# Kernel optimization log

Measured on AMD Instinct MI355X. Metric: run time of the kernel, lower is better.

Reference implementation:

```python
import jax, jax.numpy as jnp
import numpy as np

N_NODES = 100000
DIN = 512
B = 1024
T_STEPS = 6
DOUT = 512


def setup_inputs() -> dict:
    key = jax.random.key(0)
    ks = jax.random.split(key, 8)
    s = 0.02  # small init scale for numerical sanity
    x = jax.random.normal(ks[0], (N_NODES, DIN), jnp.float32)
    batch = jnp.sort(jax.random.randint(ks[1], (N_NODES,), 0, B)).astype(jnp.int64)
    Wih = jax.random.normal(ks[2], (4 * DIN, 2 * DIN), jnp.float32) * s
    Whh = jax.random.normal(ks[3], (4 * DIN, DIN), jnp.float32) * s
    bih = jax.random.normal(ks[4], (4 * DIN,), jnp.float32) * s
    bhh = jax.random.normal(ks[5], (4 * DIN,), jnp.float32) * s
    Wpost = jax.random.normal(ks[6], (DOUT, 2 * DIN), jnp.float32) * s
    bpost = jax.random.normal(ks[7], (DOUT,), jnp.float32) * s
    return {"x": x, "batch": batch, "Wih": Wih, "Whh": Whh, "bih": bih,
            "bhh": bhh, "Wpost": Wpost, "bpost": bpost, "num_graphs": B}


def reference(x, batch, Wih, Whh, bih, bhh, Wpost, bpost, num_graphs):
    din = x.shape[1]
    Bg = num_graphs
    h = jnp.zeros((Bg, din), x.dtype)
    c = jnp.zeros((Bg, din), x.dtype)
    q_star = jnp.zeros((Bg, 2 * din), x.dtype)  # [q, r]
    for _ in range(T_STEPS):
        # single-layer LSTM cell over the "batch of graphs" axis
        z = q_star @ Wih.T + h @ Whh.T + (bih + bhh)  # [B, 4*din]
        i, f, g, o = jnp.split(z, 4, axis=-1)  # torch gate order i,f,g,o
        c = jax.nn.sigmoid(f) * c + jax.nn.sigmoid(i) * jnp.tanh(g)
        h = jax.nn.sigmoid(o) * jnp.tanh(c)
        q = h  # [B, din]
        # segment (scatter) softmax attention over nodes of each graph
        e = jnp.sum(x * q[batch], axis=-1)  # [N]
        emax = jax.ops.segment_max(e, batch, num_segments=Bg)
        ex = jnp.exp(e - emax[batch])
        denom = jax.ops.segment_sum(ex, batch, num_segments=Bg)
        a = ex / denom[batch]  # [N]
        r = jax.ops.segment_sum(a[:, None] * x, batch, num_segments=Bg)  # [B, din]
        q_star = jnp.concatenate([q, r], axis=-1)
    # post_pool: Linear(2*din -> dim_out) + bias + ReLU (dropout=0, eval mode)
    out = jax.nn.relu(q_star @ Wpost.T + bpost)
    return out
```

## Files before the change

### kernel.cpp

```cpp
#include <hip/hip_runtime.h>
#include <stdint.h>
#include <stddef.h>

#define DIN    512
#define BGR    1024
#define NGATE  2048
#define KQ     1024
#define DOUT   512
#define TSTEPS 6

typedef unsigned short ushort_t;
typedef short bf16x8 __attribute__((ext_vector_type(8)));
typedef unsigned short u16x8 __attribute__((ext_vector_type(8)));
typedef float f32x4 __attribute__((ext_vector_type(4)));

__device__ __forceinline__ float b2f(unsigned short u) {
    unsigned int i = ((unsigned int)u) << 16;
    float f;
    __builtin_memcpy(&f, &i, 4);
    return f;
}

__device__ __forceinline__ unsigned short f2b(float f) {
    unsigned int i;
    __builtin_memcpy(&i, &f, 4);
    unsigned int lsb = (i >> 16) & 1u;
    i += 0x7fffu + lsb;
    return (unsigned short)(i >> 16);
}

__device__ __forceinline__ float fast_sigmoid(float v) {
    return 1.f / (1.f + __expf(-v));
}

__device__ __forceinline__ float fast_tanh(float v) {
    float t = fabsf(v);
    float e = __expf(-2.f * t);
    float r = (1.f - e) / (1.f + e);
    return v < 0.f ? -r : r;
}

__global__ void probe_dtypes(const ushort_t* x, const ushort_t* Wih,
                             const ushort_t* Whh, const ushort_t* bih,
                             const ushort_t* bhh, const ushort_t* Wpost,
                             const ushort_t* bpost, int* flags)
{
    __shared__ int cnt[7];
    const int tid = threadIdx.x;
    if (tid < 7) cnt[tid] = 0;
    __syncthreads();
    const int t = tid >> 5;
    const int l = tid & 31;
    if (t < 7) {
        const ushort_t* p = (t == 0) ? x : (t == 1) ? Wih : (t == 2) ? Whh
                          : (t == 3) ? bih : (t == 4) ? bhh
                          : (t == 5) ? Wpost : bpost;
        int good = 0;
        for (int i = 0; i < 4; i++) {
            ushort_t u = p[(l * 4 + i) * 2];
            int ex = (u >> 7) & 0xFF;
            if (ex == 0 || (ex >= 96 && ex <= 143)) good++;
        }
        atomicAdd(&cnt[t], good);
    }
    __syncthreads();
    if (tid < 7) flags[tid] = (cnt[tid] < 96) ? 1 : 0;
}

#define BM 64
#define BN 64
#define BK 32

__global__ __launch_bounds__(256)
void gemm_cell(const ushort_t* __restrict__ Ag,
               const ushort_t* __restrict__ Wg,
               const float* __restrict__ bias2,
               float* __restrict__ c, float* __restrict__ H)
{
    __shared__ __align__(16) ushort_t As[BM * BK];
    __shared__ __align__(16) ushort_t Bs[BM * BK];

    const int tid  = threadIdx.x;
    const int lane = tid & 63;
    const int w    = tid >> 6;
    const int lrow = lane & 15;
    const int quad = lane >> 4;

    const int n0 = blockIdx.x * 64;
    const int m0 = blockIdx.y * BM;

    const int srow = tid >> 2;
    const int scol = (tid & 3) * 8;

    const ushort_t* aSrc = Ag + (size_t)(m0 + srow) * KQ + scol;
    const ushort_t* bSrc = Wg + (size_t)(n0 + srow) * KQ + scol;

    f32x4 acc[4];
#pragma unroll
    for (int ni = 0; ni < 4; ni++) acc[ni] = (f32x4){0.f, 0.f, 0.f, 0.f};

    bf16x8 av = *(const bf16x8*)(aSrc);
    bf16x8 bv = *(const bf16x8*)(bSrc);

    for (int kt = 0; kt < KQ; kt += BK) {
        __syncthreads();
        *(bf16x8*)&As[srow * BK + scol] = av;
        *(bf16x8*)&Bs[srow * BK + scol] = bv;
        if (kt + BK < KQ) {
            av = *(const bf16x8*)(aSrc + kt + BK);
            bv = *(const bf16x8*)(bSrc + kt + BK);
        }
        __syncthreads();

        bf16x8 af = *(const bf16x8*)&As[(w * 16 + lrow) * BK + quad * 8];
        bf16x8 bfr[4];
#pragma unroll
        for (int ni = 0; ni < 4; ni++)
            bfr[ni] = *(const bf16x8*)&Bs[(ni * 16 + lrow) * BK + quad * 8];
#pragma unroll
        for (int ni = 0; ni < 4; ni++)
            acc[ni] = __builtin_amdgcn_mfma_f32_16x16x32_bf16(
                af, bfr[ni], acc[ni], 0, 0, 0);
    }

    const int d   = blockIdx.x * 16 + lrow;
    const float bi = bias2[n0 + lrow];
    const float bf = bias2[n0 + 16 + lrow];
    const float bg = bias2[n0 + 32 + lrow];
    const float bo = bias2[n0 + 48 + lrow];
#pragma unroll
    for (int r = 0; r < 4; r++) {
        const int gm = m0 + w * 16 + quad * 4 + r;
        float zi = acc[0][r] + bi;
        float zf = acc[1][r] + bf;
        float zg = acc[2][r] + bg;
        float zo = acc[3][r] + bo;
        size_t off = (size_t)gm * DIN + d;
        float cc = c[off];
        cc = fast_sigmoid(zf) * cc + fast_sigmoid(zi) * fast_tanh(zg);
        float hh = fast_sigmoid(zo) * fast_tanh(cc);
        c[off] = cc;
        H[off] = hh;
    }
}

template <int MODE>
__global__ __launch_bounds__(256)
void gemm_bt(const ushort_t* __restrict__ Ag, const ushort_t* __restrict__ Bg,
             const float* __restrict__ bias, float* __restrict__ Cout,
             int M, int N, int K)
{
    __shared__ __align__(16) ushort_t As[BM * BK];
    __shared__ __align__(16) ushort_t Bs[BN * BK];

    const int tid  = threadIdx.x;
    const int lane = tid & 63;
    const int w    = tid >> 6;
    const int wr   = w >> 1;
    const int wc   = w & 1;
    const int lrow = lane & 15;
    const int quad = lane >> 4;

    const int n0 = blockIdx.x * BN;
    const int m0 = blockIdx.y * BM;

    const int srow = tid >> 2;
    const int scol = (tid & 3) * 8;

    const ushort_t* aSrc = Ag + (size_t)(m0 + srow) * K + scol;
    const ushort_t* bSrc = Bg + (size_t)(n0 + srow) * K + scol;

    f32x4 acc[2][2];
#pragma unroll
    for (int i = 0; i < 2; i++)
#pragma unroll
        for (int j = 0; j < 2; j++)
            acc[i][j] = (f32x4){0.f, 0.f, 0.f, 0.f};

    bf16x8 av = *(const bf16x8*)(aSrc);
    bf16x8 bv = *(const bf16x8*)(bSrc);

    for (int kt = 0; kt < K; kt += BK) {
        __syncthreads();
        *(bf16x8*)&As[srow * BK + scol] = av;
        *(bf16x8*)&Bs[srow * BK + scol] = bv;
        if (kt + BK < K) {
            av = *(const bf16x8*)(aSrc + kt + BK);
            bv = *(const bf16x8*)(bSrc + kt + BK);
        }
        __syncthreads();

        bf16x8 af[2], bfr[2];
#pragma unroll
        for (int mi = 0; mi < 2; mi++)
            af[mi] = *(const bf16x8*)&As[(wr * 32 + mi * 16 + lrow) * BK + quad * 8];
#pragma unroll
        for (int ni = 0; ni < 2; ni++)
            bfr[ni] = *(const bf16x8*)&Bs[(wc * 32 + ni * 16 + lrow) * BK + quad * 8];

#pragma unroll
        for (int mi = 0; mi < 2; mi++)
#pragma unroll
            for (int ni = 0; ni < 2; ni++)
                acc[mi][ni] = __builtin_amdgcn_mfma_f32_16x16x32_bf16(
                    af[mi], bfr[ni], acc[mi][ni], 0, 0, 0);
    }

#pragma unroll
    for (int mi = 0; mi < 2; mi++) {
#pragma unroll
        for (int ni = 0; ni < 2; ni++) {
#pragma unroll
            for (int r = 0; r < 4; r++) {
                int gm = m0 + wr * 32 + mi * 16 + quad * 4 + r;
                int gn = n0 + wc * 32 + ni * 16 + lrow;
                float v = acc[mi][ni][r] + bias[gn];
                if (MODE == 1) {
                    if (!(v > 0.f) && (v == v)) v = 0.f;
                }
                Cout[(size_t)gm * N + gn] = v;
            }
        }
    }
}

template <int XMODE>
__global__ __launch_bounds__(256)
void attn_step(const ushort_t* __restrict__ xbsrc, const ushort_t* __restrict__ xraw,
               ushort_t* __restrict__ xbdst, const int* __restrict__ offs,
               const float* __restrict__ H, ushort_t* __restrict__ A,
               const int* __restrict__ flags)
{
    const int b    = blockIdx.x;
    const int tid  = threadIdx.x;
    const int lane = tid & 63;
    const int w    = tid >> 6;
    const int xf   = (XMODE == 0) ? 0 : flags[0];

    __shared__ float accL[4][DIN];
    __shared__ float mw[4], lw[4];

    const float* hrow = H + (size_t)b * DIN;
    {
        const int d0 = tid * 2;
        A[(size_t)b * KQ + d0]     = f2b(hrow[d0]);
        A[(size_t)b * KQ + d0 + 1] = f2b(hrow[d0 + 1]);
    }
    f32x4 q0 = *(const f32x4*)(hrow + lane * 8);
    f32x4 q1 = *(const f32x4*)(hrow + lane * 8 + 4);
    float q8[8] = {q0[0], q0[1], q0[2], q0[3], q1[0], q1[1], q1[2], q1[3]};

    const int s  = offs[b];
    const int en = offs[b + 1];

    const float NEG_INF = -__builtin_inff();
    float m = NEG_INF, l = 0.f;
    float acc[8];
#pragma unroll
    for (int j = 0; j < 8; j++) acc[j] = 0.f;

    auto load_row = [&](int n, float* v) {
        if (XMODE == 0 || !xf) {
            const ushort_t* src = (XMODE == 0) ? xbsrc : xraw;
            u16x8 xv = *(const u16x8*)(src + (size_t)n * DIN + lane * 8);
#pragma unroll
            for (int j = 0; j < 8; j++) v[j] = b2f(xv[j]);
            if (XMODE == 1)
                *(u16x8*)(xbdst + (size_t)n * DIN + lane * 8) = xv;
        } else {
            const float* xp = (const float*)xraw;
            f32x4 v0 = *(const f32x4*)(xp + (size_t)n * DIN + lane * 8);
            f32x4 v1 = *(const f32x4*)(xp + (size_t)n * DIN + lane * 8 + 4);
#pragma unroll
            for (int j = 0; j < 4; j++) { v[j] = v0[j]; v[4 + j] = v1[j]; }
            if (XMODE == 1) {
                u16x8 o;
#pragma unroll
                for (int j = 0; j < 8; j++) o[j] = f2b(v[j]);
                *(u16x8*)(xbdst + (size_t)n * DIN + lane * 8) = o;
            }
        }
    };

    auto update = [&](float e, const float* xv) {
        float mn = fmaxf(m, e);
        float al = __expf(m - mn);
        float pp = __expf(e - mn);
        l = l * al + pp;
#pragma unroll
        for (int j = 0; j < 8; j++) acc[j] = acc[j] * al + pp * xv[j];
        m = mn;
    };

    float xa[8] = {0.f}, xc[8] = {0.f};
    int n = s + w;
    if (n < en)     load_row(n, xa);
    if (n + 4 < en) load_row(n + 4, xc);
    for (; n < en; n += 8) {
        float pa[8], pc[8];
        const int np = n + 8;
        if (np < en)     load_row(np, pa);
        if (np + 4 < en) load_row(np + 4, pc);

        float e1 = 0.f, e2 = 0.f;
#pragma unroll
        for (int j = 0; j < 8; j++) { e1 += q8[j] * xa[j]; e2 += q8[j] * xc[j]; }
#pragma unroll
        for (int off = 32; off > 0; off >>= 1) {
            e1 += __shfl_xor(e1, off, 64);
            e2 += __shfl_xor(e2, off, 64);
        }

        update(e1, xa);
        if (n + 4 < en) update(e2, xc);

#pragma unroll
        for (int j = 0; j < 8; j++) { xa[j] = pa[j]; xc[j] = pc[j]; }
    }

    if (lane == 0) { mw[w] = m; lw[w] = l; }
#pragma unroll
    for (int j = 0; j < 8; j++) accL[w][lane * 8 + j] = acc[j];
    __syncthreads();

    const float M = fmaxf(fmaxf(mw[0], mw[1]), fmaxf(mw[2], mw[3]));
    const int d0 = tid * 2;
    float r0 = 0.f, r1 = 0.f, lt = 0.f;
#pragma unroll
    for (int ww = 0; ww < 4; ww++) {
        float mwv = mw[ww];
        float a = (mwv == NEG_INF) ? 0.f : __expf(mwv - M);
        lt += a * lw[ww];
        r0 += a * accL[ww][d0];
        r1 += a * accL[ww][d0 + 1];
    }
    float inv = lt > 0.f ? 1.f / lt : 0.f;
    A[(size_t)b * KQ + DIN + d0]     = f2b(r0 * inv);
    A[(size_t)b * KQ + DIN + d0 + 1] = f2b(r1 * inv);
}

__global__ void prep_weights(const ushort_t* __restrict__ Wih,
                             const ushort_t* __restrict__ Whh,
                             const ushort_t* __restrict__ bih,
                             const ushort_t* __restrict__ bhh,
                             const ushort_t* __restrict__ Wpost,
                             const ushort_t* __restrict__ bpost,
                             ushort_t* __restrict__ Wp,
                             float* __restrict__ bias2,
                             float* __restrict__ biaspost,
                             ushort_t* __restrict__ Wpb,
                             const int* __restrict__ flags)
{
    const int idx = blockIdx.x * 256 + threadIdx.x;
    const int fWih = flags[1], fWhh = flags[2], fbih = flags[3];
    const int fbhh = flags[4], fWpo = flags[5], fbpo = flags[6];

    if (idx < NGATE * KQ) {
        const int nn = idx >> 10;
        const int k  = idx & 1023;
        const int g  = (nn >> 4) & 3;
        const int n  = g * 512 + (nn >> 6) * 16 + (nn & 15);
        const int widx = n * KQ + k;
        float v = fWih ? ((const float*)Wih)[widx] : b2f(Wih[widx]);
        if (k < DIN) {
            int hidx = n * DIN + k;
            v += fWhh ? ((const float*)Whh)[hidx] : b2f(Whh[hidx]);
        }
        Wp[idx] = f2b(v);
    }
    if (idx < DOUT * KQ) {
        Wpb[idx] = fWpo ? f2b(((const float*)Wpost)[idx]) : Wpost[idx];
    }
    if (idx < NGATE) {
        const int g = (idx >> 4) & 3;
        const int n = g * 512 + (idx >> 6) * 16 + (idx & 15);
        float v1 = fbih ? ((const float*)bih)[n] : b2f(bih[n]);
        float v2 = fbhh ? ((const float*)bhh)[n] : b2f(bhh[n]);
        bias2[idx] = v1 + v2;
    }
    if (idx < DOUT) {
        biaspost[idx] = fbpo ? ((const float*)bpost)[idx] : b2f(bpost[idx]);
    }
}

__global__ void prep_h0(const ushort_t* __restrict__ bih,
                        const ushort_t* __restrict__ bhh,
                        float* __restrict__ c, float* __restrict__ H,
                        ushort_t* __restrict__ A, const int* __restrict__ flags)
{
    const int b   = blockIdx.x;
    const int tid = threadIdx.x;
    const int fbih = flags[3], fbhh = flags[4];
    for (int d = tid; d < DIN; d += 256) {
        auto ld = [&](int n) {
            float v1 = fbih ? ((const float*)bih)[n] : b2f(bih[n]);
            float v2 = fbhh ? ((const float*)bhh)[n] : b2f(bhh[n]);
            return v1 + v2;
        };
        float zi = ld(d);
        float zg = ld(2 * DIN + d);
        float zo = ld(3 * DIN + d);
        float c0 = fast_sigmoid(zi) * fast_tanh(zg);
        float h0 = fast_sigmoid(zo) * fast_tanh(c0);
        c[(size_t)b * DIN + d] = c0;
        H[(size_t)b * DIN + d] = h0;
        A[(size_t)b * KQ + d]       = f2b(h0);
        A[(size_t)b * KQ + DIN + d] = 0;
    }
}

__global__ void prep_offsets(const int* __restrict__ batch, int* __restrict__ offs, int Nn)
{
    int n = blockIdx.x * 256 + threadIdx.x;
    if (n >= Nn) return;
    const bool is64 = batch[Nn - 1] < batch[Nn - 2];
    int cur  = is64 ? batch[2 * n] : batch[n];
    int prev = (n == 0) ? -1 : (is64 ? batch[2 * (n - 1)] : batch[n - 1]);
    for (int bb = prev + 1; bb <= cur; ++bb) offs[bb] = n;
    if (n == Nn - 1) {
        for (int bb = cur + 1; bb <= BGR; ++bb) offs[bb] = Nn;
    }
}

extern "C" void kernel_launch(void* const* d_in, const int* in_sizes, int n_in,
                              void* d_out, int out_size, void* d_ws, size_t ws_size,
                              hipStream_t stream)
{
    const ushort_t* x     = (const ushort_t*)d_in[0];
    const int*      batch = (const int*)d_in[1];
    const ushort_t* Wih   = (const ushort_t*)d_in[2];
    const ushort_t* Whh   = (const ushort_t*)d_in[3];
    const ushort_t* bih   = (const ushort_t*)d_in[4];
    const ushort_t* bhh   = (const ushort_t*)d_in[5];
    const ushort_t* Wpost = (const ushort_t*)d_in[6];
    const ushort_t* bpost = (const ushort_t*)d_in[7];
    const int Nn = in_sizes[1];
    const long long Tx = (long long)in_sizes[0];

    char* p = (char*)d_ws;
    auto carve = [&](size_t bytes) -> void* {
        char* q = p;
        p += (bytes + 255) & ~(size_t)255;
        return (void*)q;
    };
    ushort_t* Wp       = (ushort_t*)carve((size_t)NGATE * KQ * 2);
    ushort_t* Wpb      = (ushort_t*)carve((size_t)DOUT * KQ * 2);
    float*    bias2    = (float*)carve((size_t)NGATE * 4);
    float*    biaspost = (float*)carve((size_t)DOUT * 4);
    float*    c        = (float*)carve((size_t)BGR * DIN * 4);
    float*    H        = (float*)carve((size_t)BGR * DIN * 4);
    ushort_t* A        = (ushort_t*)carve((size_t)BGR * KQ * 2);
    int*      offs     = (int*)carve((size_t)(BGR + 1) * 4);
    int*      flags    = (int*)carve(16 * 4);
    size_t used = (size_t)(p - (char*)d_ws);
    const bool use_xb = (ws_size >= used + (size_t)Tx * 2 + 256);
    ushort_t* xb = use_xb ? (ushort_t*)carve((size_t)Tx * 2) : nullptr;

    probe_dtypes<<<1, 256, 0, stream>>>(x, Wih, Whh, bih, bhh, Wpost, bpost, flags);
    prep_weights<<<(NGATE * KQ) / 256, 256, 0, stream>>>(
        Wih, Whh, bih, bhh, Wpost, bpost, Wp, bias2, biaspost, Wpb, flags);
    prep_h0<<<BGR, 256, 0, stream>>>(bih, bhh, c, H, A, flags);
    prep_offsets<<<(Nn + 255) / 256, 256, 0, stream>>>(batch, offs, Nn);

    for (int t = 0; t < TSTEPS; ++t) {
        if (t > 0)
            gemm_cell<<<dim3(NGATE / 64, BGR / BM), 256, 0, stream>>>(
                A, Wp, bias2, c, H);
        if (use_xb) {
            if (t == 0)
                attn_step<1><<<BGR, 256, 0, stream>>>(xb, x, xb, offs, H, A, flags);
            else
                attn_step<0><<<BGR, 256, 0, stream>>>(xb, x, xb, offs, H, A, flags);
        } else {
            attn_step<2><<<BGR, 256, 0, stream>>>(x, x, nullptr, offs, H, A, flags);
        }
    }
    gemm_bt<1><<<dim3(DOUT / BN, BGR / BM), 256, 0, stream>>>(
        A, Wpb, biaspost, (float*)d_out, BGR, DOUT, KQ);
}
```

Before: 529.3 us.

## Fuse prep kernels, use direct-to-LDS loads in cell GEMM, deepen attention pipeline

```diff
diff --git a/kernel.cpp b/kernel.cpp
--- a/kernel.cpp
+++ b/kernel.cpp
@@ -40,31 +40,12 @@
     return v < 0.f ? -r : r;
 }
 
-__global__ void probe_dtypes(const ushort_t* x, const ushort_t* Wih,
-                             const ushort_t* Whh, const ushort_t* bih,
-                             const ushort_t* bhh, const ushort_t* Wpost,
-                             const ushort_t* bpost, int* flags)
-{
-    __shared__ int cnt[7];
-    const int tid = threadIdx.x;
-    if (tid < 7) cnt[tid] = 0;
-    __syncthreads();
-    const int t = tid >> 5;
-    const int l = tid & 31;
-    if (t < 7) {
-        const ushort_t* p = (t == 0) ? x : (t == 1) ? Wih : (t == 2) ? Whh
-                          : (t == 3) ? bih : (t == 4) ? bhh
-                          : (t == 5) ? Wpost : bpost;
-        int good = 0;
-        for (int i = 0; i < 4; i++) {
-            ushort_t u = p[(l * 4 + i) * 2];
-            int ex = (u >> 7) & 0xFF;
-            if (ex == 0 || (ex >= 96 && ex <= 143)) good++;
-        }
-        atomicAdd(&cnt[t], good);
-    }
-    __syncthreads();
-    if (tid < 7) flags[tid] = (cnt[tid] < 96) ? 1 : 0;
+__device__ __forceinline__ void gld_lds16(const ushort_t* g, ushort_t* l) {
+    auto const* gp = reinterpret_cast<const unsigned int __attribute__((address_space(1)))*>(
+        reinterpret_cast<uintptr_t>(g));
+    auto* lp = reinterpret_cast<unsigned int __attribute__((address_space(3)))*>(
+        reinterpret_cast<uintptr_t>(l));
+    __builtin_amdgcn_global_load_lds(gp, lp, 16, 0, 0);
 }
 
 #define BM 64
@@ -77,8 +58,8 @@
                const float* __restrict__ bias2,
                float* __restrict__ c, float* __restrict__ H)
 {
-    __shared__ __align__(16) ushort_t As[BM * BK];
-    __shared__ __align__(16) ushort_t Bs[BM * BK];
+    __shared__ __align__(16) ushort_t As[64 * 64];
+    __shared__ __align__(16) ushort_t Bs[64 * 64];
 
     const int tid  = threadIdx.x;
     const int lane = tid & 63;
@@ -87,55 +68,62 @@
     const int quad = lane >> 4;
 
     const int n0 = blockIdx.x * 64;
-    const int m0 = blockIdx.y * BM;
-
-    const int srow = tid >> 2;
-    const int scol = (tid & 3) * 8;
-
-    const ushort_t* aSrc = Ag + (size_t)(m0 + srow) * KQ + scol;
-    const ushort_t* bSrc = Wg + (size_t)(n0 + srow) * KQ + scol;
-
-    f32x4 acc[4];
-#pragma unroll
-    for (int ni = 0; ni < 4; ni++) acc[ni] = (f32x4){0.f, 0.f, 0.f, 0.f};
-
-    bf16x8 av = *(const bf16x8*)(aSrc);
-    bf16x8 bv = *(const bf16x8*)(bSrc);
-
-    for (int kt = 0; kt < KQ; kt += BK) {
+    const int m0 = blockIdx.y * 64;
+
+    const int r8  = lane >> 3;
+    const int csw = 8 * ((lane & 7) ^ r8);
+
+    const ushort_t* aS0 = Ag + (size_t)(m0 + w * 16 + r8) * KQ + csw;
+    const ushort_t* aS1 = Ag + (size_t)(m0 + w * 16 + 8 + r8) * KQ + csw;
+    const ushort_t* bS0 = Wg + (size_t)(n0 + w * 16 + r8) * KQ + csw;
+    const ushort_t* bS1 = Wg + (size_t)(n0 + w * 16 + 8 + r8) * KQ + csw;
+    ushort_t* aL0 = As + w * 1024;
+    ushort_t* aL1 = As + w * 1024 + 512;
+    ushort_t* bL0 = Bs + w * 1024;
+    ushort_t* bL1 = Bs + w * 1024 + 512;
+
+    f32x4 acc4[4];
+#pragma unroll
+    for (int ni = 0; ni < 4; ni++) acc4[ni] = (f32x4){0.f, 0.f, 0.f, 0.f};
+
+    const int rx = lrow & 7;
+
+    for (int kt = 0; kt < KQ; kt += 64) {
         __syncthreads();
-        *(bf16x8*)&As[srow * BK + scol] = av;
-        *(bf16x8*)&Bs[srow * BK + scol] = bv;
-        if (kt + BK < KQ) {
-            av = *(const bf16x8*)(aSrc + kt + BK);
-            bv = *(const bf16x8*)(bSrc + kt + BK);
-        }
+        gld_lds16(aS0 + kt, aL0);
+        gld_lds16(aS1 + kt, aL1);
+        gld_lds16(bS0 + kt, bL0);
+        gld_lds16(bS1 + kt, bL1);
         __syncthreads();
 
-        bf16x8 af = *(const bf16x8*)&As[(w * 16 + lrow) * BK + quad * 8];
-        bf16x8 bfr[4];
-#pragma unroll
-        for (int ni = 0; ni < 4; ni++)
-            bfr[ni] = *(const bf16x8*)&Bs[(ni * 16 + lrow) * BK + quad * 8];
-#pragma unroll
-        for (int ni = 0; ni < 4; ni++)
-            acc[ni] = __builtin_amdgcn_mfma_f32_16x16x32_bf16(
-                af, bfr[ni], acc[ni], 0, 0, 0);
-    }
-
-    const int d   = blockIdx.x * 16 + lrow;
-    const float bi = bias2[n0 + lrow];
-    const float bf = bias2[n0 + 16 + lrow];
-    const float bg = bias2[n0 + 32 + lrow];
-    const float bo = bias2[n0 + 48 + lrow];
+#pragma unroll
+        for (int ks = 0; ks < 2; ks++) {
+            const int coff = 8 * ((ks * 4 + quad) ^ rx);
+            bf16x8 af = *(const bf16x8*)&As[(w * 16 + lrow) * 64 + coff];
+            bf16x8 bfr[4];
+#pragma unroll
+            for (int ni = 0; ni < 4; ni++)
+                bfr[ni] = *(const bf16x8*)&Bs[(ni * 16 + lrow) * 64 + coff];
+#pragma unroll
+            for (int ni = 0; ni < 4; ni++)
+                acc4[ni] = __builtin_amdgcn_mfma_f32_16x16x32_bf16(
+                    af, bfr[ni], acc4[ni], 0, 0, 0);
+        }
+    }
+
+    const int dd  = blockIdx.x * 16 + lrow;
+    const float bi_ = bias2[n0 + lrow];
+    const float bf_ = bias2[n0 + 16 + lrow];
+    const float bg_ = bias2[n0 + 32 + lrow];
+    const float bo_ = bias2[n0 + 48 + lrow];
 #pragma unroll
     for (int r = 0; r < 4; r++) {
         const int gm = m0 + w * 16 + quad * 4 + r;
-        float zi = acc[0][r] + bi;
-        float zf = acc[1][r] + bf;
-        float zg = acc[2][r] + bg;
-        float zo = acc[3][r] + bo;
-        size_t off = (size_t)gm * DIN + d;
+        float zi = acc4[0][r] + bi_;
+        float zf = acc4[1][r] + bf_;
+        float zg = acc4[2][r] + bg_;
+        float zo = acc4[3][r] + bo_;
+        size_t off = (size_t)gm * DIN + dd;
         float cc = c[off];
         cc = fast_sigmoid(zf) * cc + fast_sigmoid(zi) * fast_tanh(zg);
         float hh = fast_sigmoid(zo) * fast_tanh(cc);
@@ -146,7 +134,7 @@
 
 template <int MODE>
 __global__ __launch_bounds__(256)
-void gemm_bt(const ushort_t* __restrict__ Ag, const ushort_t* __restrict__ Bg,
+void gemm_bt(const ushort_t* __restrict__ Ag, const ushort_t* __restrict__ Bgm,
              const float* __restrict__ bias, float* __restrict__ Cout,
              int M, int N, int K)
 {
@@ -167,8 +155,8 @@
     const int srow = tid >> 2;
     const int scol = (tid & 3) * 8;
 
-    const ushort_t* aSrc = Ag + (size_t)(m0 + srow) * K + scol;
-    const ushort_t* bSrc = Bg + (size_t)(n0 + srow) * K + scol;
+    const ushort_t* aSrc = Ag  + (size_t)(m0 + srow) * K + scol;
+    const ushort_t* bSrc = Bgm + (size_t)(n0 + srow) * K + scol;
 
     f32x4 acc[2][2];
 #pragma unroll
@@ -225,7 +213,7 @@
 }
 
 template <int XMODE>
-__global__ __launch_bounds__(256)
+__global__ __launch_bounds__(256, 4)
 void attn_step(const ushort_t* __restrict__ xbsrc, const ushort_t* __restrict__ xraw,
                ushort_t* __restrict__ xbdst, const int* __restrict__ offs,
                const float* __restrict__ H, ushort_t* __restrict__ A,
@@ -242,13 +230,14 @@
 
     const float* hrow = H + (size_t)b * DIN;
     {
-        const int d0 = tid * 2;
-        A[(size_t)b * KQ + d0]     = f2b(hrow[d0]);
-        A[(size_t)b * KQ + d0 + 1] = f2b(hrow[d0 + 1]);
-    }
-    f32x4 q0 = *(const f32x4*)(hrow + lane * 8);
-    f32x4 q1 = *(const f32x4*)(hrow + lane * 8 + 4);
-    float q8[8] = {q0[0], q0[1], q0[2], q0[3], q1[0], q1[1], q1[2], q1[3]};
+        const int dq = tid * 2;
+        unsigned int qw = (unsigned int)f2b(hrow[dq])
+                        | ((unsigned int)f2b(hrow[dq + 1]) << 16);
+        *(unsigned int*)&A[(size_t)b * KQ + dq] = qw;
+    }
+    f32x4 q0v = *(const f32x4*)(hrow + lane * 8);
+    f32x4 q1v = *(const f32x4*)(hrow + lane * 8 + 4);
+    float q8[8] = {q0v[0], q0v[1], q0v[2], q0v[3], q1v[0], q1v[1], q1v[2], q1v[3]};
 
     const int s  = offs[b];
     const int en = offs[b + 1];
@@ -292,30 +281,45 @@
         m = mn;
     };
 
-    float xa[8] = {0.f}, xc[8] = {0.f};
+    float x0[8] = {0.f}, x1[8] = {0.f}, x2[8] = {0.f}, x3[8] = {0.f};
     int n = s + w;
-    if (n < en)     load_row(n, xa);
-    if (n + 4 < en) load_row(n + 4, xc);
-    for (; n < en; n += 8) {
-        float pa[8], pc[8];
-        const int np = n + 8;
-        if (np < en)     load_row(np, pa);
-        if (np + 4 < en) load_row(np + 4, pc);
-
-        float e1 = 0.f, e2 = 0.f;
-#pragma unroll
-        for (int j = 0; j < 8; j++) { e1 += q8[j] * xa[j]; e2 += q8[j] * xc[j]; }
+    if (n < en)      load_row(n, x0);
+    if (n + 4 < en)  load_row(n + 4, x1);
+    if (n + 8 < en)  load_row(n + 8, x2);
+    if (n + 12 < en) load_row(n + 12, x3);
+    for (; n < en; n += 16) {
+        float p0[8], p1[8], p2[8], p3[8];
+        const int np = n + 16;
+        if (np < en)      load_row(np, p0);
+        if (np + 4 < en)  load_row(np + 4, p1);
+        if (np + 8 < en)  load_row(np + 8, p2);
+        if (np + 12 < en) load_row(np + 12, p3);
+
+        float e0 = 0.f, e1 = 0.f, e2 = 0.f, e3 = 0.f;
+#pragma unroll
+        for (int j = 0; j < 8; j++) {
+            e0 += q8[j] * x0[j];
+            e1 += q8[j] * x1[j];
+            e2 += q8[j] * x2[j];
+            e3 += q8[j] * x3[j];
+        }
 #pragma unroll
         for (int off = 32; off > 0; off >>= 1) {
+            e0 += __shfl_xor(e0, off, 64);
             e1 += __shfl_xor(e1, off, 64);
             e2 += __shfl_xor(e2, off, 64);
-        }
-
-        update(e1, xa);
-        if (n + 4 < en) update(e2, xc);
-
-#pragma unroll
-        for (int j = 0; j < 8; j++) { xa[j] = pa[j]; xc[j] = pc[j]; }
+            e3 += __shfl_xor(e3, off, 64);
+        }
+
+        update(e0, x0);
+        if (n + 4 < en)  update(e1, x1);
+        if (n + 8 < en)  update(e2, x2);
+        if (n + 12 < en) update(e3, x3);
+
+#pragma unroll
+        for (int j = 0; j < 8; j++) {
+            x0[j] = p0[j]; x1[j] = p1[j]; x2[j] = p2[j]; x3[j] = p3[j];
+        }
     }
 
     if (lane == 0) { mw[w] = m; lw[w] = l; }
@@ -335,25 +339,58 @@
         r1 += a * accL[ww][d0 + 1];
     }
     float inv = lt > 0.f ? 1.f / lt : 0.f;
-    A[(size_t)b * KQ + DIN + d0]     = f2b(r0 * inv);
-    A[(size_t)b * KQ + DIN + d0 + 1] = f2b(r1 * inv);
-}
-
-__global__ void prep_weights(const ushort_t* __restrict__ Wih,
-                             const ushort_t* __restrict__ Whh,
-                             const ushort_t* __restrict__ bih,
-                             const ushort_t* __restrict__ bhh,
-                             const ushort_t* __restrict__ Wpost,
-                             const ushort_t* __restrict__ bpost,
-                             ushort_t* __restrict__ Wp,
-                             float* __restrict__ bias2,
-                             float* __restrict__ biaspost,
-                             ushort_t* __restrict__ Wpb,
-                             const int* __restrict__ flags)
+    unsigned int rw = (unsigned int)f2b(r0 * inv)
+                    | ((unsigned int)f2b(r1 * inv) << 16);
+    *(unsigned int*)&A[(size_t)b * KQ + DIN + d0] = rw;
+}
+
+__global__ void prep_all(const ushort_t* __restrict__ x,
+                         const ushort_t* __restrict__ Wih,
+                         const ushort_t* __restrict__ Whh,
+                         const ushort_t* __restrict__ bih,
+                         const ushort_t* __restrict__ bhh,
+                         const ushort_t* __restrict__ Wpost,
+                         const ushort_t* __restrict__ bpost,
+                         const int* __restrict__ batch, int Nn,
+                         ushort_t* __restrict__ Wp,
+                         float* __restrict__ bias2,
+                         float* __restrict__ biaspost,
+                         ushort_t* __restrict__ Wpb,
+                         float* __restrict__ c,
+                         float* __restrict__ H,
+                         ushort_t* __restrict__ A,
+                         int* __restrict__ offs,
+                         int* __restrict__ flags)
 {
-    const int idx = blockIdx.x * 256 + threadIdx.x;
-    const int fWih = flags[1], fWhh = flags[2], fbih = flags[3];
-    const int fbhh = flags[4], fWpo = flags[5], fbpo = flags[6];
+    __shared__ int cnt[7];
+    __shared__ int fsh[7];
+    const int tid = threadIdx.x;
+    if (tid < 7) cnt[tid] = 0;
+    __syncthreads();
+    {
+        const int t = tid >> 5;
+        const int l = tid & 31;
+        if (t < 7) {
+            const ushort_t* pp = (t == 0) ? x : (t == 1) ? Wih : (t == 2) ? Whh
+                               : (t == 3) ? bih : (t == 4) ? bhh
+                               : (t == 5) ? Wpost : bpost;
+            int good = 0;
+            for (int i = 0; i < 4; i++) {
+                ushort_t u = pp[(l * 4 + i) * 2];
+                int ex = (u >> 7) & 0xFF;
+                if (ex == 0 || (ex >= 96 && ex <= 143)) good++;
+            }
+            atomicAdd(&cnt[t], good);
+        }
+    }
+    __syncthreads();
+    if (tid < 7) fsh[tid] = (cnt[tid] < 96) ? 1 : 0;
+    __syncthreads();
+    const int fWih = fsh[1], fWhh = fsh[2], fbih = fsh[3];
+    const int fbhh = fsh[4], fWpo = fsh[5], fbpo = fsh[6];
+
+    const int idx = blockIdx.x * 256 + tid;
+    if (blockIdx.x == 0 && tid < 7) flags[tid] = fsh[tid];
 
     if (idx < NGATE * KQ) {
         const int nn = idx >> 10;
@@ -381,44 +418,32 @@
     if (idx < DOUT) {
         biaspost[idx] = fbpo ? ((const float*)bpost)[idx] : b2f(bpost[idx]);
     }
-}
-
-__global__ void prep_h0(const ushort_t* __restrict__ bih,
-                        const ushort_t* __restrict__ bhh,
-                        float* __restrict__ c, float* __restrict__ H,
-                        ushort_t* __restrict__ A, const int* __restrict__ flags)
-{
-    const int b   = blockIdx.x;
-    const int tid = threadIdx.x;
-    const int fbih = flags[3], fbhh = flags[4];
-    for (int d = tid; d < DIN; d += 256) {
-        auto ld = [&](int n) {
-            float v1 = fbih ? ((const float*)bih)[n] : b2f(bih[n]);
-            float v2 = fbhh ? ((const float*)bhh)[n] : b2f(bhh[n]);
-            return v1 + v2;
-        };
-        float zi = ld(d);
-        float zg = ld(2 * DIN + d);
-        float zo = ld(3 * DIN + d);
+
+    if (idx < BGR * DIN) {
+        const int d = idx & (DIN - 1);
+        float zi = fbih ? ((const float*)bih)[d] : b2f(bih[d]);
+        zi      += fbhh ? ((const float*)bhh)[d] : b2f(bhh[d]);
+        float zg = fbih ? ((const float*)bih)[2 * DIN + d] : b2f(bih[2 * DIN + d]);
+        zg      += fbhh ? ((const float*)bhh)[2 * DIN + d] : b2f(bhh[2 * DIN + d]);
+        float zo = fbih ? ((const float*)bih)[3 * DIN + d] : b2f(bih[3 * DIN + d]);
+        zo      += fbhh ? ((const float*)bhh)[3 * DIN + d] : b2f(bhh[3 * DIN + d]);
         float c0 = fast_sigmoid(zi) * fast_tanh(zg);
         float h0 = fast_sigmoid(zo) * fast_tanh(c0);
-        c[(size_t)b * DIN + d] = c0;
-        H[(size_t)b * DIN + d] = h0;
-        A[(size_t)b * KQ + d]       = f2b(h0);
-        A[(size_t)b * KQ + DIN + d] = 0;
-    }
-}
-
-__global__ void prep_offsets(const int* __restrict__ batch, int* __restrict__ offs, int Nn)
-{
-    int n = blockIdx.x * 256 + threadIdx.x;
-    if (n >= Nn) return;
-    const bool is64 = batch[Nn - 1] < batch[Nn - 2];
-    int cur  = is64 ? batch[2 * n] : batch[n];
-    int prev = (n == 0) ? -1 : (is64 ? batch[2 * (n - 1)] : batch[n - 1]);
-    for (int bb = prev + 1; bb <= cur; ++bb) offs[bb] = n;
-    if (n == Nn - 1) {
-        for (int bb = cur + 1; bb <= BGR; ++bb) offs[bb] = Nn;
+        c[idx] = c0;
+        H[idx] = h0;
+        const int bg = idx >> 9;
+        A[(size_t)bg * KQ + d]       = f2b(h0);
+        A[(size_t)bg * KQ + DIN + d] = 0;
+    }
+
+    if (idx < Nn) {
+        const bool is64 = batch[Nn - 1] < batch[Nn - 2];
+        int cur  = is64 ? batch[2 * idx] : batch[idx];
+        int prev = (idx == 0) ? -1 : (is64 ? batch[2 * (idx - 1)] : batch[idx - 1]);
+        for (int bb = prev + 1; bb <= cur; ++bb) offs[bb] = idx;
+        if (idx == Nn - 1) {
+            for (int bb = cur + 1; bb <= BGR; ++bb) offs[bb] = Nn;
+        }
     }
 }
 
@@ -456,15 +481,13 @@
     const bool use_xb = (ws_size >= used + (size_t)Tx * 2 + 256);
     ushort_t* xb = use_xb ? (ushort_t*)carve((size_t)Tx * 2) : nullptr;
 
-    probe_dtypes<<<1, 256, 0, stream>>>(x, Wih, Whh, bih, bhh, Wpost, bpost, flags);
-    prep_weights<<<(NGATE * KQ) / 256, 256, 0, stream>>>(
-        Wih, Whh, bih, bhh, Wpost, bpost, Wp, bias2, biaspost, Wpb, flags);
-    prep_h0<<<BGR, 256, 0, stream>>>(bih, bhh, c, H, A, flags);
-    prep_offsets<<<(Nn + 255) / 256, 256, 0, stream>>>(batch, offs, Nn);
+    prep_all<<<(NGATE * KQ) / 256, 256, 0, stream>>>(
+        x, Wih, Whh, bih, bhh, Wpost, bpost, batch, Nn,
+        Wp, bias2, biaspost, Wpb, c, H, A, offs, flags);
 
     for (int t = 0; t < TSTEPS; ++t) {
         if (t > 0)
-            gemm_cell<<<dim3(NGATE / 64, BGR / BM), 256, 0, stream>>>(
+            gemm_cell<<<dim3(NGATE / 64, BGR / 64), 256, 0, stream>>>(
                 A, Wp, bias2, c, H);
         if (use_xb) {
             if (t == 0)
```

Result: no change. 530.6 us (+0.2%).
